# Performance work log

Measured on AMD Instinct MI355X. Metric: run time of the kernel, lower is better.

## Reference

```python
import jax, jax.numpy as jnp
import numpy as np

N = 50000          # num nodes
E = 800000         # num edges (avg degree 16)
R = 8              # num relations
IN = 128
H0 = 256
H1 = 64


def _w(key, shape, fan_in):
    return jax.random.normal(key, shape, dtype=jnp.float32) * (1.0 / np.sqrt(fan_in))


def setup_inputs() -> dict:
    key = jax.random.key(0)
    ks = jax.random.split(key, 16)
    x = jax.random.normal(ks[0], (N, IN), dtype=jnp.float32)
    edge_index = jax.random.randint(ks[1], (2, E), 0, N, dtype=jnp.int64)
    edge_type = jax.random.randint(ks[2], (E,), 0, R, dtype=jnp.int64)
    return {
        "x": x,
        "edge_index": edge_index,
        "edge_type": edge_type,
        # RGCNConv params: per-relation weights [R, in, out], root weight [in, out], bias [out]
        "W1": _w(ks[3], (R, IN, H0), IN), "root1": _w(ks[4], (IN, H0), IN), "b1": jnp.zeros((H0,), jnp.float32),
        "W2": _w(ks[5], (R, H0, H0), H0), "root2": _w(ks[6], (H0, H0), H0), "b2": jnp.zeros((H0,), jnp.float32),
        "W3": _w(ks[7], (R, H0, H0), H0), "root3": _w(ks[8], (H0, H0), H0), "b3": jnp.zeros((H0,), jnp.float32),
        "W4": _w(ks[9], (R, H0, H1), H0), "root4": _w(ks[10], (H0, H1), H0), "b4": jnp.zeros((H1,), jnp.float32),
    }


def rgcn_layer(x, edge_index, edge_type, W, root, bias):
    """PyG RGCNConv: out_i = x_i @ root + sum_r (1/|N_r(i)|) sum_{j in N_r(i)} x_j @ W_r + bias.
    Aggregation is linear, so aggregate source features per (relation, dst) first,
    then apply the R small GEMMs — avoids per-edge [E, out] message materialization."""
    src, dst = edge_index[0], edge_index[1]
    seg = edge_type * N + dst                      # combined (relation, dst) segment id
    nseg = R * N
    agg = jax.ops.segment_sum(x[src], seg, num_segments=nseg)          # [R*N, in]
    cnt = jax.ops.segment_sum(jnp.ones((seg.shape[0],), x.dtype), seg, num_segments=nseg)
    agg = agg / jnp.maximum(cnt, 1.0)[:, None]                          # mean per (r, i)
    agg = agg.reshape(R, N, x.shape[1])                                 # [R, N, in]
    return jnp.einsum('rni,rio->no', agg, W) + x @ root + bias


def reference(x, edge_index, edge_type, W1, root1, b1, W2, root2, b2, W3, root3, b3, W4, root4, b4):
    h = jax.nn.relu(rgcn_layer(x, edge_index, edge_type, W1, root1, b1))
    h = jax.nn.relu(rgcn_layer(h, edge_index, edge_type, W2, root2, b2))
    h = jax.nn.relu(rgcn_layer(h, edge_index, edge_type, W3, root3, b3))
    return rgcn_layer(h, edge_index, edge_type, W4, root4, b4)
```

## Files before the change

kernel.cpp:

```cpp
#include <hip/hip_runtime.h>

#define N_NODES 50000
#define N_PAD   50048
#define N_EDGES 800000
#define N_REL   8
#define NSEG    (N_REL * N_NODES)
#define SCAN_NB 391
#define NSTRIPE 391
#define SPX     49

typedef short bf16x8 __attribute__((ext_vector_type(8)));
typedef float f32x4  __attribute__((ext_vector_type(4)));

__device__ __forceinline__ ushort f2bf(float f) {
    union { float f; unsigned u; } c; c.f = f;
    unsigned u = c.u + 0x7fffu + ((c.u >> 16) & 1u);
    return (ushort)(u >> 16);
}
__device__ __forceinline__ void add8(float* s, uint4 v) {
    unsigned u[4] = {v.x, v.y, v.z, v.w};
    #pragma unroll
    for (int k = 0; k < 4; ++k) {
        s[2 * k]     += __uint_as_float(u[k] << 16);
        s[2 * k + 1] += __uint_as_float(u[k] & 0xffff0000u);
    }
}
__device__ __forceinline__ void async16(const ushort* g, ushort* l) {
    __builtin_amdgcn_global_load_lds((const __attribute__((address_space(1))) void*)g,
                                     (__attribute__((address_space(3))) void*)l, 16, 0, 0);
}


__global__ void count_edges(const int* __restrict__ dst, const int* __restrict__ et,
                            int* __restrict__ cnt) {
    int e = blockIdx.x * 256 + threadIdx.x;
    if (e < N_EDGES) atomicAdd(&cnt[et[e] * N_NODES + dst[e]], 1);
}

__global__ __launch_bounds__(256) void scan_pass1(const int* __restrict__ cnt,
                                                  int* __restrict__ sums) {
    __shared__ int sc[256];
    int b = blockIdx.x, t = threadIdx.x;
    int base = b * 1024 + t * 4;
    int v = 0;
    #pragma unroll
    for (int i = 0; i < 4; ++i) { int idx = base + i; if (idx < NSEG) v += cnt[idx]; }
    sc[t] = v; __syncthreads();
    for (int off = 1; off < 256; off <<= 1) {
        int x = (t >= off) ? sc[t - off] : 0;
        __syncthreads(); sc[t] += x; __syncthreads();
    }
    if (t == 255) sums[b] = sc[255];
}

__global__ __launch_bounds__(512) void scan_pass2(int* __restrict__ sums, int nb) {
    __shared__ int sc[512];
    int t = threadIdx.x;
    int v = (t < nb) ? sums[t] : 0;
    sc[t] = v; __syncthreads();
    for (int off = 1; off < 512; off <<= 1) {
        int x = (t >= off) ? sc[t - off] : 0;
        __syncthreads(); sc[t] += x; __syncthreads();
    }
    if (t < nb) sums[t] = sc[t] - v;
}

__global__ __launch_bounds__(256) void scan_pass3(const int* __restrict__ cnt,
                                                  const int* __restrict__ sums,
                                                  int* __restrict__ row_ptr) {
    __shared__ int sc[256];
    int b = blockIdx.x, t = threadIdx.x;
    int base = b * 1024 + t * 4;
    int e[4]; int v = 0;
    #pragma unroll
    for (int i = 0; i < 4; ++i) { int idx = base + i; e[i] = (idx < NSEG) ? cnt[idx] : 0; v += e[i]; }
    sc[t] = v; __syncthreads();
    for (int off = 1; off < 256; off <<= 1) {
        int x = (t >= off) ? sc[t - off] : 0;
        __syncthreads(); sc[t] += x; __syncthreads();
    }
    int run = sums[b] + (sc[t] - v);
    #pragma unroll
    for (int i = 0; i < 4; ++i) {
        int idx = base + i;
        if (idx < NSEG) row_ptr[idx] = run;
        run += e[i];
    }
    if (b == 0 && t == 0) row_ptr[NSEG] = N_EDGES;
}

__global__ void place_edges(const int* __restrict__ src, const int* __restrict__ dst,
                            const int* __restrict__ et, const int* __restrict__ row_ptr,
                            int* __restrict__ cnt, int* __restrict__ sorted_src) {
    int e = blockIdx.x * 256 + threadIdx.x;
    if (e >= N_EDGES) return;
    int key = et[e] * N_NODES + dst[e];
    int old = atomicSub(&cnt[key], 1);
    sorted_src[row_ptr[key] + old - 1] = src[e];
}


__global__ void convert_weights(const float* __restrict__ W, const float* __restrict__ root,
                                ushort* __restrict__ BT, int K, int O, int NPAD) {
    int idx = blockIdx.x * 256 + threadIdx.x;
    if (idx >= NPAD * K) return;
    int col = idx / K, i = idx % K;
    float v = 0.0f;
    if (col < N_REL * O) {
        int r = col / O, o = col % O;
        v = W[((size_t)r * K + i) * O + o];
    } else if (col < (N_REL + 1) * O) {
        v = root[(size_t)i * O + (col - N_REL * O)];
    }
    BT[idx] = f2bf(v);
}

__global__ void f32_to_bf16(const float* __restrict__ in, ushort* __restrict__ out, int n4) {
    int i = blockIdx.x * 256 + threadIdx.x;
    if (i >= n4) return;
    float4 v = ((const float4*)in)[i];
    ushort4 s; s.x = f2bf(v.x); s.y = f2bf(v.y); s.z = f2bf(v.z); s.w = f2bf(v.w);
    ((ushort4*)out)[i] = s;
}

template<int K, int CTS>
__global__ __launch_bounds__(256)
void gemm_mfma(const ushort* __restrict__ A, const ushort* __restrict__ BT,
               ushort* __restrict__ Y, int NW) {
    const int f = blockIdx.x;
    const int g = f & 7, m = f >> 3;
    const int y = g + 8 * (m / CTS);
    const int ct = m % CTS;
    if (y >= NSTRIPE) return;
    const int row0 = y * 128;
    const int col0 = ct * 128;

    __shared__ ushort SMEM[9216];
    ushort* As = SMEM;
    ushort* Bs = SMEM + 4096;
    const int t = threadIdx.x;
    const int lane = t & 63;
    const int w = t >> 6;
    const int l16 = lane & 15, q = lane >> 4;
    const int wm = (w & 1) * 64, wn = (w >> 1) * 64;

    const int c0i = w * 64 + lane;
    const int c1i = c0i + 256;
    const size_t ga0 = (size_t)(c0i >> 2) * K + (size_t)(c0i & 3) * 8;
    const size_t ga1 = (size_t)(c1i >> 2) * K + (size_t)(c1i & 3) * 8;
    const ushort* Ab = A + (size_t)row0 * K;
    const ushort* Bb = BT + (size_t)col0 * K;
    ushort* lA0 = &As[w * 512];
    ushort* lA1 = &As[(w + 4) * 512];
    ushort* lB0 = &Bs[w * 512];
    ushort* lB1 = &Bs[(w + 4) * 512];

    f32x4 acc[4][4] = {};

    #pragma unroll
    for (int k0 = 0; k0 < K; k0 += 32) {
        __syncthreads();
        async16(Ab + k0 + ga0, lA0);
        async16(Ab + k0 + ga1, lA1);
        async16(Bb + k0 + ga0, lB0);
        async16(Bb + k0 + ga1, lB1);
        __syncthreads();
        bf16x8 a[4], b[4];
        #pragma unroll
        for (int i = 0; i < 4; ++i) {
            a[i] = *(const bf16x8*)&As[(wm + i * 16 + l16) * 32 + q * 8];
            b[i] = *(const bf16x8*)&Bs[(wn + i * 16 + l16) * 32 + q * 8];
        }
        #pragma unroll
        for (int i = 0; i < 4; ++i)
            #pragma unroll
            for (int j = 0; j < 4; ++j)
                acc[i][j] = __builtin_amdgcn_mfma_f32_16x16x32_bf16(a[i], b[j], acc[i][j], 0, 0, 0);
    }

    __syncthreads();
    ushort* Ts = &SMEM[w * 32 * 72];
    const int rr = lane >> 3;
    const int cc = (lane & 7) * 8;
    #pragma unroll
    for (int half = 0; half < 2; ++half) {
        #pragma unroll
        for (int i = 0; i < 2; ++i)
            #pragma unroll
            for (int j = 0; j < 4; ++j)
                #pragma unroll
                for (int r = 0; r < 4; ++r)
                    Ts[(i * 16 + q * 4 + r) * 72 + j * 16 + l16] = f2bf(acc[half * 2 + i][j][r]);
        #pragma unroll
        for (int p = 0; p < 4; ++p) {
            int row = p * 8 + rr;
            uint4 v = *(const uint4*)&Ts[row * 72 + cc];
            *(uint4*)(Y + (size_t)(row0 + wm + half * 32 + row) * NW + col0 + wn + cc) = v;
        }
    }
}

template<int O>
__global__ __launch_bounds__(256)
void gather_kernel(const ushort* __restrict__ Y, int NW,
                   const int* __restrict__ row_ptr, const int* __restrict__ sorted_src,
                   const float* __restrict__ bias,
                   float* __restrict__ out_f32, ushort* __restrict__ out_bf16, int relu) {
    constexpr int TPN = O / 8;
    int d = blockIdx.x * (256 / TPN) + threadIdx.x / TPN;
    if (d >= N_NODES) return;
    int c0 = (threadIdx.x % TPN) * 8;
    int s0[N_REL], s1[N_REL];
    #pragma unroll
    for (int r = 0; r < N_REL; ++r) {
        s0[r] = row_ptr[r * N_NODES + d];
        s1[r] = row_ptr[r * N_NODES + d + 1];
    }
    float sum[8] = {};
    add8(sum, *(const uint4*)(Y + (size_t)d * NW + N_REL * O + c0));
    #pragma unroll
    for (int k = 0; k < 8; ++k) sum[k] += bias[c0 + k];
    for (int r = 0; r < N_REL; ++r) {
        if (s1[r] <= s0[r]) continue;
        float ps[8] = {};
        const ushort* Yc = Y + r * O + c0;
        for (int e = s0[r]; e < s1[r]; ++e)
            add8(ps, *(const uint4*)(Yc + (size_t)sorted_src[e] * NW));
        float inv = 1.0f / (float)(s1[r] - s0[r]);
        #pragma unroll
        for (int k = 0; k < 8; ++k) sum[k] += ps[k] * inv;
    }
    if (relu) {
        #pragma unroll
        for (int k = 0; k < 8; ++k) sum[k] = fmaxf(sum[k], 0.0f);
    }
    if (out_bf16) {
        ushort o[8];
        #pragma unroll
        for (int k = 0; k < 8; ++k) o[k] = f2bf(sum[k]);
        *(uint4*)(out_bf16 + (size_t)d * O + c0) = *(const uint4*)o;
    } else {
        float* p = out_f32 + (size_t)d * O + c0;
        *(float4*)p = make_float4(sum[0], sum[1], sum[2], sum[3]);
        *(float4*)(p + 4) = make_float4(sum[4], sum[5], sum[6], sum[7]);
    }
}


extern "C" void kernel_launch(void* const* d_in, const int* in_sizes, int n_in,
                              void* d_out, int out_size, void* d_ws, size_t ws_size,
                              hipStream_t stream) {
    const float* x  = (const float*)d_in[0];
    const int*   ei = (const int*)d_in[1];
    const int*   et = (const int*)d_in[2];
    const float* W[4]  = {(const float*)d_in[3], (const float*)d_in[6], (const float*)d_in[9],  (const float*)d_in[12]};
    const float* RT[4] = {(const float*)d_in[4], (const float*)d_in[7], (const float*)d_in[10], (const float*)d_in[13]};
    const float* BI[4] = {(const float*)d_in[5], (const float*)d_in[8], (const float*)d_in[11], (const float*)d_in[14]};
    const int KS[4] = {128, 256, 256, 256};
    const int NP[4] = {2304, 2304, 2304, 640};
    const int* src = ei;
    const int* dst = ei + N_EDGES;

    char* ws = (char*)d_ws;
    size_t off = 0;
    auto take = [&](size_t bytes) -> char* {
        char* p = ws + off;
        off = (off + bytes + 255) & ~(size_t)255;
        return p;
    };
    int* cnt        = (int*)take((size_t)NSEG * 4);
    int* row_ptr    = (int*)take((size_t)(NSEG + 1) * 4);
    int* sums       = (int*)take(512 * 4);
    int* sorted_src = (int*)take((size_t)N_EDGES * 4);
    ushort* BTp[4];
    for (int l = 0; l < 4; ++l) BTp[l] = (ushort*)take((size_t)NP[l] * KS[l] * 2);
    ushort* hb = (ushort*)take((size_t)N_PAD * 256 * 2);
    ushort* Yb = (ushort*)take((size_t)N_PAD * 2304 * 2);

    hipMemsetAsync(cnt, 0, (size_t)NSEG * 4, stream);
    count_edges<<<(N_EDGES + 255) / 256, 256, 0, stream>>>(dst, et, cnt);
    scan_pass1<<<SCAN_NB, 256, 0, stream>>>(cnt, sums);
    scan_pass2<<<1, 512, 0, stream>>>(sums, SCAN_NB);
    scan_pass3<<<SCAN_NB, 256, 0, stream>>>(cnt, sums, row_ptr);
    place_edges<<<(N_EDGES + 255) / 256, 256, 0, stream>>>(src, dst, et, row_ptr, cnt, sorted_src);

    for (int l = 0; l < 4; ++l) {
        int n = NP[l] * KS[l];
        convert_weights<<<(n + 255) / 256, 256, 0, stream>>>(W[l], RT[l], BTp[l], KS[l], 
                                                             l == 3 ? 64 : 256, NP[l]);
    }

    f32_to_bf16<<<(N_NODES * 128 / 4 + 255) / 256, 256, 0, stream>>>(x, hb, N_NODES * 128 / 4);

    const int G18 = 8 * SPX * 18;
    const int G5  = 8 * SPX * 5;
    gemm_mfma<128, 18><<<G18, 256, 0, stream>>>(hb, BTp[0], Yb, 2304);
    gather_kernel<256><<<dim3((N_NODES + 7) / 8), 256, 0, stream>>>(
        Yb, 2304, row_ptr, sorted_src, BI[0], nullptr, hb, 1);

    gemm_mfma<256, 18><<<G18, 256, 0, stream>>>(hb, BTp[1], Yb, 2304);
    gather_kernel<256><<<dim3((N_NODES + 7) / 8), 256, 0, stream>>>(
        Yb, 2304, row_ptr, sorted_src, BI[1], nullptr, hb, 1);

    gemm_mfma<256, 18><<<G18, 256, 0, stream>>>(hb, BTp[2], Yb, 2304);
    gather_kernel<256><<<dim3((N_NODES + 7) / 8), 256, 0, stream>>>(
        Yb, 2304, row_ptr, sorted_src, BI[2], nullptr, hb, 1);

    gemm_mfma<256, 5><<<G5, 256, 0, stream>>>(hb, BTp[3], Yb, 640);
    gather_kernel<64><<<dim3((N_NODES + 31) / 32), 256, 0, stream>>>(
        Yb, 640, row_ptr, sorted_src, BI[3], (float*)d_out, nullptr, 0);
}
```

Measured before the change: 732.3 us.

## Reorder CSR by destination, pack edge metadata, unroll gather, direct GEMM stores

Segments are now keyed by (dst, relation) instead of (relation, dst), so each node's edges across all relations form one contiguous range. Each sorted edge entry packs the source id, relation and segment count into one int, which lets the gather read only two row_ptr values and run a single 4-way unrolled loop with FMA-weighted accumulation. The GEMM swaps MFMA operands so each lane holds four consecutive output columns and writes them straight to global memory, dropping the LDS transpose epilogue. The count and sum scratch buffers alias the Y buffer to save workspace. The bit packing assumes node ids below 2^17 and per-segment counts below 4096, and the direct GEMM stores are narrower (8-byte) than the previous 16-byte ones.

```diff
diff --git a/kernel.cpp b/kernel.cpp
--- a/kernel.cpp
+++ b/kernel.cpp
@@ -25,6 +25,14 @@
         s[2 * k + 1] += __uint_as_float(u[k] & 0xffff0000u);
     }
 }
+__device__ __forceinline__ void fma8(float* s, uint4 v, float w) {
+    unsigned u[4] = {v.x, v.y, v.z, v.w};
+    #pragma unroll
+    for (int k = 0; k < 4; ++k) {
+        s[2 * k]     = fmaf(__uint_as_float(u[k] << 16),        w, s[2 * k]);
+        s[2 * k + 1] = fmaf(__uint_as_float(u[k] & 0xffff0000u), w, s[2 * k + 1]);
+    }
+}
 __device__ __forceinline__ void async16(const ushort* g, ushort* l) {
     __builtin_amdgcn_global_load_lds((const __attribute__((address_space(1))) void*)g,
                                      (__attribute__((address_space(3))) void*)l, 16, 0, 0);
@@ -34,7 +42,7 @@
 __global__ void count_edges(const int* __restrict__ dst, const int* __restrict__ et,
                             int* __restrict__ cnt) {
     int e = blockIdx.x * 256 + threadIdx.x;
-    if (e < N_EDGES) atomicAdd(&cnt[et[e] * N_NODES + dst[e]], 1);
+    if (e < N_EDGES) atomicAdd(&cnt[dst[e] * N_REL + et[e]], 1);
 }
 
 __global__ __launch_bounds__(256) void scan_pass1(const int* __restrict__ cnt,
@@ -91,12 +99,15 @@
 
 __global__ void place_edges(const int* __restrict__ src, const int* __restrict__ dst,
                             const int* __restrict__ et, const int* __restrict__ row_ptr,
-                            int* __restrict__ cnt, int* __restrict__ sorted_src) {
+                            int* __restrict__ cnt, int* __restrict__ sorted) {
     int e = blockIdx.x * 256 + threadIdx.x;
     if (e >= N_EDGES) return;
-    int key = et[e] * N_NODES + dst[e];
+    int r = et[e];
+    int key = dst[e] * N_REL + r;
     int old = atomicSub(&cnt[key], 1);
-    sorted_src[row_ptr[key] + old - 1] = src[e];
+    int r0 = row_ptr[key];
+    int c = row_ptr[key + 1] - r0;
+    sorted[r0 + old - 1] = src[e] | (r << 17) | (c << 20);
 }
 
 
@@ -123,10 +134,10 @@
     ((ushort4*)out)[i] = s;
 }
 
-template<int K, int CTS>
+template<int K, int CTS, int NW>
 __global__ __launch_bounds__(256)
 void gemm_mfma(const ushort* __restrict__ A, const ushort* __restrict__ BT,
-               ushort* __restrict__ Y, int NW) {
+               ushort* __restrict__ Y) {
     const int f = blockIdx.x;
     const int g = f & 7, m = f >> 3;
     const int y = g + 8 * (m / CTS);
@@ -135,7 +146,7 @@
     const int row0 = y * 128;
     const int col0 = ct * 128;
 
-    __shared__ ushort SMEM[9216];
+    __shared__ ushort SMEM[8192];
     ushort* As = SMEM;
     ushort* Bs = SMEM + 4096;
     const int t = threadIdx.x;
@@ -175,27 +186,18 @@
         for (int i = 0; i < 4; ++i)
             #pragma unroll
             for (int j = 0; j < 4; ++j)
-                acc[i][j] = __builtin_amdgcn_mfma_f32_16x16x32_bf16(a[i], b[j], acc[i][j], 0, 0, 0);
-    }
-
-    __syncthreads();
-    ushort* Ts = &SMEM[w * 32 * 72];
-    const int rr = lane >> 3;
-    const int cc = (lane & 7) * 8;
-    #pragma unroll
-    for (int half = 0; half < 2; ++half) {
-        #pragma unroll
-        for (int i = 0; i < 2; ++i)
-            #pragma unroll
-            for (int j = 0; j < 4; ++j)
-                #pragma unroll
-                for (int r = 0; r < 4; ++r)
-                    Ts[(i * 16 + q * 4 + r) * 72 + j * 16 + l16] = f2bf(acc[half * 2 + i][j][r]);
-        #pragma unroll
-        for (int p = 0; p < 4; ++p) {
-            int row = p * 8 + rr;
-            uint4 v = *(const uint4*)&Ts[row * 72 + cc];
-            *(uint4*)(Y + (size_t)(row0 + wm + half * 32 + row) * NW + col0 + wn + cc) = v;
+                acc[i][j] = __builtin_amdgcn_mfma_f32_16x16x32_bf16(b[j], a[i], acc[i][j], 0, 0, 0);
+    }
+
+    #pragma unroll
+    for (int i = 0; i < 4; ++i) {
+        const size_t rbase = (size_t)(row0 + wm + i * 16 + l16) * NW + col0 + wn + q * 4;
+        #pragma unroll
+        for (int j = 0; j < 4; ++j) {
+            uint2 v;
+            v.x = (unsigned)f2bf(acc[i][j][0]) | ((unsigned)f2bf(acc[i][j][1]) << 16);
+            v.y = (unsigned)f2bf(acc[i][j][2]) | ((unsigned)f2bf(acc[i][j][3]) << 16);
+            *(uint2*)(Y + rbase + j * 16) = v;
         }
     }
 }
@@ -203,33 +205,41 @@
 template<int O>
 __global__ __launch_bounds__(256)
 void gather_kernel(const ushort* __restrict__ Y, int NW,
-                   const int* __restrict__ row_ptr, const int* __restrict__ sorted_src,
+                   const int* __restrict__ row_ptr, const int* __restrict__ sorted,
                    const float* __restrict__ bias,
                    float* __restrict__ out_f32, ushort* __restrict__ out_bf16, int relu) {
     constexpr int TPN = O / 8;
     int d = blockIdx.x * (256 / TPN) + threadIdx.x / TPN;
     if (d >= N_NODES) return;
     int c0 = (threadIdx.x % TPN) * 8;
-    int s0[N_REL], s1[N_REL];
-    #pragma unroll
-    for (int r = 0; r < N_REL; ++r) {
-        s0[r] = row_ptr[r * N_NODES + d];
-        s1[r] = row_ptr[r * N_NODES + d + 1];
-    }
+    int p0 = row_ptr[d * N_REL];
+    int p1 = row_ptr[d * N_REL + N_REL];
     float sum[8] = {};
     add8(sum, *(const uint4*)(Y + (size_t)d * NW + N_REL * O + c0));
     #pragma unroll
     for (int k = 0; k < 8; ++k) sum[k] += bias[c0 + k];
-    for (int r = 0; r < N_REL; ++r) {
-        if (s1[r] <= s0[r]) continue;
-        float ps[8] = {};
-        const ushort* Yc = Y + r * O + c0;
-        for (int e = s0[r]; e < s1[r]; ++e)
-            add8(ps, *(const uint4*)(Yc + (size_t)sorted_src[e] * NW));
-        float inv = 1.0f / (float)(s1[r] - s0[r]);
-        #pragma unroll
-        for (int k = 0; k < 8; ++k) sum[k] += ps[k] * inv;
-    }
+    const ushort* Yc = Y + c0;
+    #define EDGE_LD(sx) (*(const uint4*)(Yc + (size_t)((sx) & 0x1FFFF) * NW + ((((sx) >> 17) & 7) * O)))
+    #define EDGE_W(sx)  (1.0f / (float)((unsigned)(sx) >> 20))
+    int e = p0;
+    for (; e + 4 <= p1; e += 4) {
+        int s0 = sorted[e], s1 = sorted[e + 1], s2 = sorted[e + 2], s3 = sorted[e + 3];
+        uint4 v0 = EDGE_LD(s0);
+        uint4 v1 = EDGE_LD(s1);
+        uint4 v2 = EDGE_LD(s2);
+        uint4 v3 = EDGE_LD(s3);
+        fma8(sum, v0, EDGE_W(s0));
+        fma8(sum, v1, EDGE_W(s1));
+        fma8(sum, v2, EDGE_W(s2));
+        fma8(sum, v3, EDGE_W(s3));
+    }
+    for (; e < p1; ++e) {
+        int s = sorted[e];
+        uint4 v = EDGE_LD(s);
+        fma8(sum, v, EDGE_W(s));
+    }
+    #undef EDGE_LD
+    #undef EDGE_W
     if (relu) {
         #pragma unroll
         for (int k = 0; k < 8; ++k) sum[k] = fmaxf(sum[k], 0.0f);
@@ -268,25 +278,25 @@
         off = (off + bytes + 255) & ~(size_t)255;
         return p;
     };
-    int* cnt        = (int*)take((size_t)NSEG * 4);
     int* row_ptr    = (int*)take((size_t)(NSEG + 1) * 4);
-    int* sums       = (int*)take(512 * 4);
-    int* sorted_src = (int*)take((size_t)N_EDGES * 4);
+    int* sorted     = (int*)take((size_t)N_EDGES * 4);
     ushort* BTp[4];
     for (int l = 0; l < 4; ++l) BTp[l] = (ushort*)take((size_t)NP[l] * KS[l] * 2);
     ushort* hb = (ushort*)take((size_t)N_PAD * 256 * 2);
     ushort* Yb = (ushort*)take((size_t)N_PAD * 2304 * 2);
+    int* cnt  = (int*)Yb;
+    int* sums = (int*)((char*)Yb + (size_t)NSEG * 4);
 
     hipMemsetAsync(cnt, 0, (size_t)NSEG * 4, stream);
     count_edges<<<(N_EDGES + 255) / 256, 256, 0, stream>>>(dst, et, cnt);
     scan_pass1<<<SCAN_NB, 256, 0, stream>>>(cnt, sums);
     scan_pass2<<<1, 512, 0, stream>>>(sums, SCAN_NB);
     scan_pass3<<<SCAN_NB, 256, 0, stream>>>(cnt, sums, row_ptr);
-    place_edges<<<(N_EDGES + 255) / 256, 256, 0, stream>>>(src, dst, et, row_ptr, cnt, sorted_src);
+    place_edges<<<(N_EDGES + 255) / 256, 256, 0, stream>>>(src, dst, et, row_ptr, cnt, sorted);
 
     for (int l = 0; l < 4; ++l) {
         int n = NP[l] * KS[l];
-        convert_weights<<<(n + 255) / 256, 256, 0, stream>>>(W[l], RT[l], BTp[l], KS[l], 
+        convert_weights<<<(n + 255) / 256, 256, 0, stream>>>(W[l], RT[l], BTp[l], KS[l],
                                                              l == 3 ? 64 : 256, NP[l]);
     }
 
@@ -294,19 +304,19 @@
 
     const int G18 = 8 * SPX * 18;
     const int G5  = 8 * SPX * 5;
-    gemm_mfma<128, 18><<<G18, 256, 0, stream>>>(hb, BTp[0], Yb, 2304);
+    gemm_mfma<128, 18, 2304><<<G18, 256, 0, stream>>>(hb, BTp[0], Yb);
     gather_kernel<256><<<dim3((N_NODES + 7) / 8), 256, 0, stream>>>(
-        Yb, 2304, row_ptr, sorted_src, BI[0], nullptr, hb, 1);
-
-    gemm_mfma<256, 18><<<G18, 256, 0, stream>>>(hb, BTp[1], Yb, 2304);
+        Yb, 2304, row_ptr, sorted, BI[0], nullptr, hb, 1);
+
+    gemm_mfma<256, 18, 2304><<<G18, 256, 0, stream>>>(hb, BTp[1], Yb);
     gather_kernel<256><<<dim3((N_NODES + 7) / 8), 256, 0, stream>>>(
-        Yb, 2304, row_ptr, sorted_src, BI[1], nullptr, hb, 1);
-
-    gemm_mfma<256, 18><<<G18, 256, 0, stream>>>(hb, BTp[2], Yb, 2304);
+        Yb, 2304, row_ptr, sorted, BI[1], nullptr, hb, 1);
+
+    gemm_mfma<256, 18, 2304><<<G18, 256, 0, stream>>>(hb, BTp[2], Yb);
     gather_kernel<256><<<dim3((N_NODES + 7) / 8), 256, 0, stream>>>(
-        Yb, 2304, row_ptr, sorted_src, BI[2], nullptr, hb, 1);
-
-    gemm_mfma<256, 5><<<G5, 256, 0, stream>>>(hb, BTp[3], Yb, 640);
+        Yb, 2304, row_ptr, sorted, BI[2], nullptr, hb, 1);
+
+    gemm_mfma<256, 5, 640><<<G5, 256, 0, stream>>>(hb, BTp[3], Yb);
     gather_kernel<64><<<dim3((N_NODES + 31) / 32), 256, 0, stream>>>(
-        Yb, 640, row_ptr, sorted_src, BI[3], (float*)d_out, nullptr, 0);
-}
+        Yb, 640, row_ptr, sorted, BI[3], (float*)d_out, nullptr, 0);
+}
```

After: 776.6 us. 6.0% more time.
